# Kernel optimization log

Hardware: AMD Instinct MI355X
Metric: run time of the kernel (lower is better)

## Reference

```python
import jax, jax.numpy as jnp
import numpy as np

EPS = 1e-5

def _quant_w(w):
    # symmetric per-tensor 8-bit weight quantization with straight-through estimator
    s = jnp.max(jnp.abs(w)) / 127.0
    wq = jnp.round(jnp.clip(w / s, -127.0, 127.0)) * s
    return w + jax.lax.stop_gradient(wq - w)

def _adder_conv(x, w, stride):
    # AdderNet conv: out[b,co,ow] = -sum_{cin,k} |x[b,cin,ow*stride+k] - w[co,cin,k]|
    # x: (B, Cin, L), w: (Co, Cin, K)
    B, Cin, L = x.shape
    Co, _, K = w.shape
    Ow = (L - K) // stride + 1
    idx = jnp.arange(Ow)[:, None] * stride + jnp.arange(K)[None, :]      # (Ow, K)
    patches = x[:, :, idx]                                               # (B, Cin, Ow, K)
    diff = jnp.abs(patches[:, None] - w[None, :, :, None, :])            # (B, Co, Cin, Ow, K)
    return -diff.sum(axis=(2, 4))                                        # (B, Co, Ow)

def _bn(x, p):
    # eval-mode BatchNorm; x: (B,C,W), p: (4,C) = [gamma, beta, running_mean, running_var]
    g, b, m, v = p
    return (x - m[:, None]) * (g[:, None] * jax.lax.rsqrt(v[:, None] + EPS)) + b[:, None]

def _bn_params(key, c):
    k1, k2, k3, k4 = jax.random.split(key, 4)
    g = jax.random.uniform(k1, (c,)) + 0.5
    b = 0.1 * jax.random.normal(k2, (c,))
    m = 0.1 * jax.random.normal(k3, (c,))
    v = jax.random.uniform(k4, (c,)) + 0.5
    return jnp.stack([g, b, m, v]).astype(jnp.float32)

def setup_inputs() -> dict:
    key = jax.random.key(0)
    ks = jax.random.split(key, 22)
    B = 8192
    w = lambda k, shp: (0.1 * jax.random.normal(k, shp)).astype(jnp.float32)
    return {
        'x': jax.random.normal(ks[0], (B, 1, 1, 256), dtype=jnp.float32),
        'w_pre1': w(ks[1], (5, 1, 13)),   'bn_pre1': _bn_params(ks[2], 5),
        'w_pre2': w(ks[3], (10, 5, 9)),   'bn_pre2': _bn_params(ks[4], 10),
        'w_r1':   w(ks[5], (10, 10, 1)),  'bn_r1':   _bn_params(ks[6], 10),
        'w_r2':   w(ks[7], (10, 10, 1)),  'bn_r2':   _bn_params(ks[8], 10),
        'w_o1a':  w(ks[9], (70, 140, 1)), 'bn_o1a':  _bn_params(ks[10], 70),
        'w_o1b':  w(ks[11], (30, 70, 1)), 'bn_o1b':  _bn_params(ks[12], 30),
        'w_o1c':  w(ks[13], (1, 30, 1)),  'bn_o1c':  _bn_params(ks[14], 1),
        'w_o2a':  w(ks[15], (70, 140, 1)),'bn_o2a':  _bn_params(ks[16], 70),
        'w_o2b':  w(ks[17], (30, 70, 1)), 'bn_o2b':  _bn_params(ks[18], 30),
        'w_o2c':  w(ks[19], (1, 30, 1)),  'bn_o2c':  _bn_params(ks[20], 1),
    }

def reference(x, w_pre1, bn_pre1, w_pre2, bn_pre2, w_r1, bn_r1, w_r2, bn_r2,
              w_o1a, bn_o1a, w_o1b, bn_o1b, w_o1c, bn_o1c,
              w_o2a, bn_o2a, w_o2b, bn_o2b, w_o2c, bn_o2c):
    relu = jax.nn.relu
    B = x.shape[0]
    h = x.reshape(B, 1, 256)                                  # height dim is 1 -> 1D
    h = relu(_bn(_adder_conv(h, _quant_w(w_pre1), 5), bn_pre1))   # (B,5,49)
    h = relu(_bn(_adder_conv(h, _quant_w(w_pre2), 3), bn_pre2))   # (B,10,14)
    # ResBlock
    t = relu(_bn(_adder_conv(h, _quant_w(w_r1), 1), bn_r1))
    t = _bn(_adder_conv(t, _quant_w(w_r2), 1), bn_r2)
    h = relu(t + h)                                           # (B,10,14)
    f = h.reshape(B, 140, 1)                                  # flatten to channels
    # O1 branch (amplitude-weighted average lifetime)
    a = relu(_bn(_adder_conv(f, _quant_w(w_o1a), 1), bn_o1a))
    a = relu(_bn(_adder_conv(a, _quant_w(w_o1b), 1), bn_o1b))
    a = relu(_bn(_adder_conv(a, _quant_w(w_o1c), 1), bn_o1c))
    tau_amp = a.reshape(-1)                                   # (B,)
    # O2 branch (intensity-weighted average lifetime)
    b = relu(_bn(_adder_conv(f, _quant_w(w_o2a), 1), bn_o2a))
    b = relu(_bn(_adder_conv(b, _quant_w(w_o2b), 1), bn_o2b))
    b = relu(_bn(_adder_conv(b, _quant_w(w_o2c), 1), bn_o2c))
    tau_inten = b.reshape(-1)                                 # (B,)
    return (tau_amp, tau_inten)
```

## Files before the change

### kernel.cpp

```cpp
#include <hip/hip_runtime.h>

#define TPB 256
#define EPB 8
#define H1S 246
#define ES  280

#define WQ1   0
#define WQ2   65
#define WR1Q  515
#define WR2Q  615
#define WCQ   715
#define WSB   779
#define SMALL_N 1253
#define WQAT  1280
#define WQBT  20880

#define SB_P1 0
#define SB_P2 10
#define SB_R1 30
#define SB_R2 50
#define SB_A1 70
#define SB_B1 210
#define SB_C1 270
#define SB_A2 272
#define SB_B2 412
#define SB_C2 472

#define GFOLD(bn, C, OFF)                                                     \
  if (tid < (C)) {                                                            \
    float gg = (bn)[tid], bb = (bn)[(C) + tid];                               \
    float mm = (bn)[2 * (C) + tid], vv = (bn)[3 * (C) + tid];                 \
    float sc = gg / sqrtf(vv + 1e-5f);                                        \
    sbp[(OFF) + tid] = sc;                                                    \
    sbp[(OFF) + (C) + tid] = bb - mm * sc;                                    \
  }

extern "C" __global__ __launch_bounds__(256)
void prep(const float* __restrict__ w1,  const float* __restrict__ bnp1,
          const float* __restrict__ w2,  const float* __restrict__ bnp2,
          const float* __restrict__ wr1, const float* __restrict__ bnr1,
          const float* __restrict__ wr2, const float* __restrict__ bnr2,
          const float* __restrict__ wa1, const float* __restrict__ bna1,
          const float* __restrict__ wb1, const float* __restrict__ bnb1,
          const float* __restrict__ wc1, const float* __restrict__ bnc1,
          const float* __restrict__ wa2, const float* __restrict__ bna2,
          const float* __restrict__ wb2, const float* __restrict__ bnb2,
          const float* __restrict__ wc2, const float* __restrict__ bnc2,
          float* __restrict__ ws)
{
  __shared__ float s_red[4];
  const int tid = threadIdx.x;
  const int b = blockIdx.x;

  if (b == 10) {
    float* sbp = ws + WSB;
    GFOLD(bnp1, 5, SB_P1)  GFOLD(bnp2, 10, SB_P2)
    GFOLD(bnr1, 10, SB_R1) GFOLD(bnr2, 10, SB_R2)
    GFOLD(bna1, 70, SB_A1) GFOLD(bnb1, 30, SB_B1) GFOLD(bnc1, 1, SB_C1)
    GFOLD(bna2, 70, SB_A2) GFOLD(bnb2, 30, SB_B2) GFOLD(bnc2, 1, SB_C2)
    return;
  }

  const float* src; int n; int mode; int rofs; float* dst = ws;
  int ofs = 0;
  switch (b) {
    case 0: src = w1;  ofs = WQ1;      n = 65;   mode = 0; rofs = 0;  break;
    case 1: src = w2;  ofs = WQ2;      n = 450;  mode = 0; rofs = 0;  break;
    case 2: src = wr1; ofs = WR1Q;     n = 100;  mode = 0; rofs = 0;  break;
    case 3: src = wr2; ofs = WR2Q;     n = 100;  mode = 0; rofs = 0;  break;
    case 4: src = wa1; ofs = WQAT;     n = 9800; mode = 1; rofs = 0;  break;
    case 5: src = wb1; ofs = WQBT;     n = 2100; mode = 2; rofs = 0;  break;
    case 6: src = wc1; ofs = WCQ;      n = 30;   mode = 0; rofs = 0;  break;
    case 7: src = wa2; ofs = WQAT;     n = 9800; mode = 1; rofs = 70; break;
    case 8: src = wb2; ofs = WQBT;     n = 2100; mode = 2; rofs = 30; break;
    default:src = wc2; ofs = WCQ + 32; n = 30;   mode = 0; rofs = 0;  break;
  }

  const int n4 = n >> 2;
  const float4* s4 = (const float4*)src;

  float m = 0.f;
  for (int i = tid; i < n4; i += 256) {
    float4 v = s4[i];
    m = fmaxf(m, fmaxf(fmaxf(fabsf(v.x), fabsf(v.y)),
                       fmaxf(fabsf(v.z), fabsf(v.w))));
  }
  for (int i = (n4 << 2) + tid; i < n; i += 256) m = fmaxf(m, fabsf(src[i]));
#pragma unroll
  for (int off = 32; off > 0; off >>= 1)
    m = fmaxf(m, __shfl_down(m, off, 64));
  if ((tid & 63) == 0) s_red[tid >> 6] = m;
  __syncthreads();
  m = fmaxf(fmaxf(s_red[0], s_red[1]), fmaxf(s_red[2], s_red[3]));

  const float s = m / 127.0f;
  auto qz = [&](float w) {
    return rintf(fminf(fmaxf(w / s, -127.f), 127.f)) * s;
  };

  if (mode == 0) {
    for (int i = tid; i < n4; i += 256) {
      float4 v = s4[i];
      int base = 4 * i;
      dst[ofs + base]     = qz(v.x);
      dst[ofs + base + 1] = qz(v.y);
      dst[ofs + base + 2] = qz(v.z);
      dst[ofs + base + 3] = qz(v.w);
    }
    for (int i = (n4 << 2) + tid; i < n; i += 256) dst[ofs + i] = qz(src[i]);
  } else if (mode == 1) {
    for (int i = tid; i < n4; i += 256) {
      float4 v = s4[i];
      int base = 4 * i;
      int r = base / 140 + rofs, c = base % 140;
      float4 q4;
      q4.x = qz(v.x); q4.y = qz(v.y); q4.z = qz(v.z); q4.w = qz(v.w);
      *(float4*)&dst[ofs + ((c >> 2) * 140 + r) * 4] = q4;
    }
  } else {
    for (int i = tid; i < n4; i += 256) {
      float4 v = s4[i];
      int base = 4 * i;
      float q[4] = {qz(v.x), qz(v.y), qz(v.z), qz(v.w)};
#pragma unroll
      for (int cpt = 0; cpt < 4; ++cpt) {
        int ii = base + cpt;
        int r = ii / 70 + rofs, c = ii % 70;
        dst[ofs + ((c >> 1) * 60 + r) * 2 + (c & 1)] = q[cpt];
      }
    }
  }
}

extern "C" __global__ __launch_bounds__(TPB, 4)
void taunet(const float* __restrict__ x, const float* __restrict__ ws,
            float* __restrict__ out, int B)
{
  __shared__ __align__(16) float s_h1[EPB * H1S];
  __shared__ __align__(16) float s_e[EPB * ES];
  __shared__ __align__(16) float s_small[SMALL_N];

  const int tid = threadIdx.x;
  const int g  = tid >> 5;
  const int l  = tid & 31;
  const int ln = tid & 63;
  const int wv = tid >> 6;
  const int gp = 2 * wv;
  const int elem = blockIdx.x * EPB + g;

  {
    const float4* w4p = (const float4*)ws;
    for (int i = ln; i < (SMALL_N >> 2); i += 64)
      *(float4*)&s_small[i * 4] = w4p[i];
    if (ln == 0) s_small[1252] = ws[1252];
  }

  {
    const float4* xb = (const float4*)x;
#pragma unroll
    for (int it = 0; it < 2; ++it) {
      int e = gp + it;
      int ge = blockIdx.x * EPB + e;
      if (ge < B) {
        float4 v = xb[ge * 64 + ln];
        *(float4*)&s_e[e * ES + ln * 4] = v;
      }
    }
  }

  const float* sb = &s_small[WSB];

  {
    const float* xe = &s_e[g * ES];
#pragma unroll
    for (int rep = 0; rep < 2; ++rep) {
      int p = l + 32 * rep;
      bool act = p < 49;
      int ps = act ? p : 0;
      float win[13];
#pragma unroll
      for (int k = 0; k < 13; ++k) win[k] = xe[5 * ps + k];
#pragma unroll
      for (int ci = 0; ci < 5; ++ci) {
        float a0 = 0.f, a1 = 0.f;
#pragma unroll
        for (int k = 0; k < 13; ++k) {
          float d = fabsf(win[k] - ws[WQ1 + ci * 13 + k]);
          if (k & 1) a1 += d; else a0 += d;
        }
        float v = fmaxf(fmaf(-(a0 + a1), ws[WSB + SB_P1 + ci],
                             ws[WSB + SB_P1 + 5 + ci]), 0.f);
        if (act) s_h1[g * H1S + ci * 49 + ps] = v;
      }
    }
  }

  {
    const int ch = l >> 4;
    const int ow16 = l & 15;
    const bool act = ow16 < 14;
    const int ow = act ? ow16 : 0;
    const float* h1b = &s_h1[g * H1S];
    float acc[5] = {0.f, 0.f, 0.f, 0.f, 0.f};
#pragma unroll
    for (int ci = 0; ci < 5; ++ci) {
      float w9[9];
#pragma unroll
      for (int k = 0; k < 9; ++k) w9[k] = h1b[ci * 49 + 3 * ow + k];
#pragma unroll
      for (int c = 0; c < 5; ++c) {
        int co = ch * 5 + c;
        float s0 = 0.f, s1 = 0.f;
#pragma unroll
        for (int k = 0; k < 9; ++k) {
          float d = fabsf(w9[k] - s_small[WQ2 + co * 45 + ci * 9 + k]);
          if (k & 1) s1 += d; else s0 += d;
        }
        acc[c] += s0 + s1;
      }
    }
#pragma unroll
    for (int c = 0; c < 5; ++c) {
      int co = ch * 5 + c;
      float v = fmaxf(fmaf(-acc[c], sb[SB_P2 + co], sb[SB_P2 + 10 + co]), 0.f);
      if (act) s_e[g * ES + co * 14 + ow] = v;
    }
  }

#pragma unroll
  for (int j = 0; j < 5; ++j) {
    int idx = l + 32 * j;
    if (idx < 140) {
      int co = idx / 14, ow = idx % 14;
      float a0 = 0.f, a1 = 0.f;
#pragma unroll
      for (int ci = 0; ci < 10; ++ci) {
        float d = fabsf(s_e[g * ES + ci * 14 + ow] - s_small[WR1Q + co * 10 + ci]);
        if (ci & 1) a1 += d; else a0 += d;
      }
      s_e[g * ES + 140 + idx] =
          fmaxf(fmaf(-(a0 + a1), sb[SB_R1 + co], sb[SB_R1 + 10 + co]), 0.f);
    }
  }

#pragma unroll
  for (int j = 0; j < 5; ++j) {
    int idx = l + 32 * j;
    if (idx < 140) {
      int co = idx / 14, ow = idx % 14;
      float a0 = 0.f, a1 = 0.f;
#pragma unroll
      for (int ci = 0; ci < 10; ++ci) {
        float d = fabsf(s_e[g * ES + 140 + ci * 14 + ow] - s_small[WR2Q + co * 10 + ci]);
        if (ci & 1) a1 += d; else a0 += d;
      }
      float t2 = fmaf(-(a0 + a1), sb[SB_R2 + co], sb[SB_R2 + 10 + co]);
      s_e[g * ES + idx] = fmaxf(t2 + s_e[g * ES + idx], 0.f);
    }
  }

  __syncthreads();

  {
    const int rh = wv >> 1;
    const int eh = wv & 1;
    const int e0 = eh * 4;
    const int rbase = rh * 70;
    const float* hbp[4] = {&s_e[(e0 + 0) * ES], &s_e[(e0 + 1) * ES],
                           &s_e[(e0 + 2) * ES], &s_e[(e0 + 3) * ES]};
    const int q1 = ln / 6;
    const int rm = ln - q1 * 6;
    const bool act1 = ln < 24;
    const int row1 = rbase + 64 + (act1 ? rm : 0);
    const float* hb1p = hbp[act1 ? q1 : 0];

    float acc0[4][4], acc1[4];
#pragma unroll
    for (int e = 0; e < 4; ++e)
#pragma unroll
      for (int j = 0; j < 4; ++j) acc0[e][j] = 0.f;
#pragma unroll
    for (int j = 0; j < 4; ++j) acc1[j] = 0.f;

#pragma unroll 2
    for (int cb = 0; cb < 35; ++cb) {
      float4 w0 = *(const float4*)&ws[WQAT + (cb * 140 + rbase + ln) * 4];
      float4 w1 = *(const float4*)&ws[WQAT + (cb * 140 + row1) * 4];
#pragma unroll
      for (int e = 0; e < 4; ++e) {
        float4 h4 = *(const float4*)&hbp[e][cb * 4];
        acc0[e][0] += fabsf(h4.x - w0.x);
        acc0[e][1] += fabsf(h4.y - w0.y);
        acc0[e][2] += fabsf(h4.z - w0.z);
        acc0[e][3] += fabsf(h4.w - w0.w);
      }
      float4 p4 = *(const float4*)&hb1p[cb * 4];
      acc1[0] += fabsf(p4.x - w1.x);
      acc1[1] += fabsf(p4.y - w1.y);
      acc1[2] += fabsf(p4.z - w1.z);
      acc1[3] += fabsf(p4.w - w1.w);
    }

    {
      int off = rh ? SB_A2 : SB_A1;
      float sc = sb[off + ln], bi = sb[off + 70 + ln];
#pragma unroll
      for (int e = 0; e < 4; ++e) {
        float sad = (acc0[e][0] + acc0[e][1]) + (acc0[e][2] + acc0[e][3]);
        s_h1[(e0 + e) * H1S + rbase + ln] = fmaxf(fmaf(-sad, sc, bi), 0.f);
      }
    }
    if (act1) {
      int off = rh ? SB_A2 : SB_A1;
      int co = 64 + rm;
      float sc = sb[off + co], bi = sb[off + 70 + co];
      float sad = (acc1[0] + acc1[1]) + (acc1[2] + acc1[3]);
      s_h1[(e0 + q1) * H1S + rbase + 64 + rm] = fmaxf(fmaf(-sad, sc, bi), 0.f);
    }
  }

  __syncthreads();

  {
    const int brh = wv >> 1;
    const int e0 = (wv & 1) * 4;
    const bool act = ln < 30;
    const int rl = act ? ln : 0;
    const int rr = brh * 30 + rl;
    const float* h0p = &s_h1[(e0 + 0) * H1S + brh * 70];
    const float* h1p = &s_h1[(e0 + 1) * H1S + brh * 70];
    const float* h2p = &s_h1[(e0 + 2) * H1S + brh * 70];
    const float* h3p = &s_h1[(e0 + 3) * H1S + brh * 70];
    const int off = brh ? SB_B2 : SB_B1;
    float a0 = 0.f, a1 = 0.f, b0 = 0.f, b1 = 0.f,
          c0 = 0.f, c1 = 0.f, d0 = 0.f, d1 = 0.f;
#pragma unroll 7
    for (int ci = 0; ci < 35; ++ci) {
      float2 w2v = *(const float2*)&ws[WQBT + (ci * 60 + rr) * 2];
      float2 h0v = *(const float2*)&h0p[2 * ci];
      float2 h1v = *(const float2*)&h1p[2 * ci];
      float2 h2v = *(const float2*)&h2p[2 * ci];
      float2 h3v = *(const float2*)&h3p[2 * ci];
      a0 += fabsf(h0v.x - w2v.x);  a1 += fabsf(h0v.y - w2v.y);
      b0 += fabsf(h1v.x - w2v.x);  b1 += fabsf(h1v.y - w2v.y);
      c0 += fabsf(h2v.x - w2v.x);  c1 += fabsf(h2v.y - w2v.y);
      d0 += fabsf(h3v.x - w2v.x);  d1 += fabsf(h3v.y - w2v.y);
    }
    if (act) {
      float sc = sb[off + rl], bi = sb[off + 30 + rl];
      s_e[(e0 + 0) * ES + 140 + rr] = fmaxf(fmaf(-(a0 + a1), sc, bi), 0.f);
      s_e[(e0 + 1) * ES + 140 + rr] = fmaxf(fmaf(-(b0 + b1), sc, bi), 0.f);
      s_e[(e0 + 2) * ES + 140 + rr] = fmaxf(fmaf(-(c0 + c1), sc, bi), 0.f);
      s_e[(e0 + 3) * ES + 140 + rr] = fmaxf(fmaf(-(d0 + d1), sc, bi), 0.f);
    }
  }

  __syncthreads();

  for (int br = 0; br < 2; ++br) {
    float d = 0.f;
    if (l < 30)
      d = fabsf(s_e[g * ES + 140 + br * 30 + l] - s_small[WCQ + br * 32 + l]);
#pragma unroll
    for (int off = 16; off > 0; off >>= 1)
      d += __shfl_down(d, off, 32);
    if (l == 0 && elem < B) {
      int sbC = br ? SB_C2 : SB_C1;
      out[br * B + elem] = fmaxf(fmaf(-d, sb[sbC], sb[sbC + 1]), 0.f);
    }
  }
}

extern "C" void kernel_launch(void* const* d_in, const int* in_sizes, int n_in,
                              void* d_out, int out_size, void* d_ws, size_t ws_size,
                              hipStream_t stream) {
  const float* x    = (const float*)d_in[0];
  const float* w1   = (const float*)d_in[1];
  const float* bnp1 = (const float*)d_in[2];
  const float* w2   = (const float*)d_in[3];
  const float* bnp2 = (const float*)d_in[4];
  const float* wr1  = (const float*)d_in[5];
  const float* bnr1 = (const float*)d_in[6];
  const float* wr2  = (const float*)d_in[7];
  const float* bnr2 = (const float*)d_in[8];
  const float* wa1  = (const float*)d_in[9];
  const float* bna1 = (const float*)d_in[10];
  const float* wb1  = (const float*)d_in[11];
  const float* bnb1 = (const float*)d_in[12];
  const float* wc1  = (const float*)d_in[13];
  const float* bnc1 = (const float*)d_in[14];
  const float* wa2  = (const float*)d_in[15];
  const float* bna2 = (const float*)d_in[16];
  const float* wb2  = (const float*)d_in[17];
  const float* bnb2 = (const float*)d_in[18];
  const float* wc2  = (const float*)d_in[19];
  const float* bnc2 = (const float*)d_in[20];

  float* ws = (float*)d_ws;
  int B = in_sizes[0] / 256;
  int blocks = (B + EPB - 1) / EPB;

  hipLaunchKernelGGL(prep, dim3(11), dim3(256), 0, stream,
                     w1, bnp1, w2, bnp2, wr1, bnr1, wr2, bnr2,
                     wa1, bna1, wb1, bnb1, wc1, bnc1,
                     wa2, bna2, wb2, bnb2, wc2, bnc2, ws);

  hipLaunchKernelGGL(taunet, dim3(blocks), dim3(TPB), 0, stream,
                     x, ws, (float*)d_out, B);
}
```

Baseline: 137.0 us.

## Halve elements per block and remap threads to one wavefront per element

Cuts the batch elements per block from 8 to 4 and gives each 64-lane wavefront one element in the early conv stages, instead of one 32-lane half-wave per element. The dense stages are re-split so each thread handles two elements, or one element for the second layer, rather than four. Launch bounds request 8 blocks per SM to raise occupancy. The trade-off is that each weight value loaded from global memory in the dense layers is now reused across fewer elements, so weight traffic per element roughly doubles, and lanes sit idle in stages 2 and 3.

```diff
diff --git a/kernel.cpp b/kernel.cpp
--- a/kernel.cpp
+++ b/kernel.cpp
@@ -1,7 +1,7 @@
 #include <hip/hip_runtime.h>
 
 #define TPB 256
-#define EPB 8
+#define EPB 4
 #define H1S 246
 #define ES  280
 
@@ -132,7 +132,7 @@
   }
 }
 
-extern "C" __global__ __launch_bounds__(TPB, 4)
+extern "C" __global__ __launch_bounds__(TPB, 8)
 void taunet(const float* __restrict__ x, const float* __restrict__ ws,
             float* __restrict__ out, int B)
 {
@@ -141,12 +141,9 @@
   __shared__ __align__(16) float s_small[SMALL_N];
 
   const int tid = threadIdx.x;
-  const int g  = tid >> 5;
-  const int l  = tid & 31;
   const int ln = tid & 63;
   const int wv = tid >> 6;
-  const int gp = 2 * wv;
-  const int elem = blockIdx.x * EPB + g;
+  const int elem = blockIdx.x * EPB + wv;
 
   {
     const float4* w4p = (const float4*)ws;
@@ -155,107 +152,102 @@
     if (ln == 0) s_small[1252] = ws[1252];
   }
 
-  {
+  if (elem < B) {
     const float4* xb = (const float4*)x;
-#pragma unroll
-    for (int it = 0; it < 2; ++it) {
-      int e = gp + it;
-      int ge = blockIdx.x * EPB + e;
-      if (ge < B) {
-        float4 v = xb[ge * 64 + ln];
-        *(float4*)&s_e[e * ES + ln * 4] = v;
-      }
-    }
+    float4 v = xb[elem * 64 + ln];
+    *(float4*)&s_e[wv * ES + ln * 4] = v;
   }
 
   const float* sb = &s_small[WSB];
 
   {
-    const float* xe = &s_e[g * ES];
-#pragma unroll
-    for (int rep = 0; rep < 2; ++rep) {
-      int p = l + 32 * rep;
-      bool act = p < 49;
-      int ps = act ? p : 0;
-      float win[13];
-#pragma unroll
-      for (int k = 0; k < 13; ++k) win[k] = xe[5 * ps + k];
-#pragma unroll
-      for (int ci = 0; ci < 5; ++ci) {
-        float a0 = 0.f, a1 = 0.f;
-#pragma unroll
-        for (int k = 0; k < 13; ++k) {
-          float d = fabsf(win[k] - ws[WQ1 + ci * 13 + k]);
-          if (k & 1) a1 += d; else a0 += d;
-        }
-        float v = fmaxf(fmaf(-(a0 + a1), ws[WSB + SB_P1 + ci],
-                             ws[WSB + SB_P1 + 5 + ci]), 0.f);
-        if (act) s_h1[g * H1S + ci * 49 + ps] = v;
-      }
-    }
-  }
-
-  {
-    const int ch = l >> 4;
-    const int ow16 = l & 15;
+    const float* xe = &s_e[wv * ES];
+    const bool act = ln < 49;
+    const int ps = act ? ln : 0;
+    float win[13];
+#pragma unroll
+    for (int k = 0; k < 13; ++k) win[k] = xe[5 * ps + k];
+#pragma unroll
+    for (int ci = 0; ci < 5; ++ci) {
+      float a0 = 0.f, a1 = 0.f;
+#pragma unroll
+      for (int k = 0; k < 13; ++k) {
+        float d = fabsf(win[k] - ws[WQ1 + ci * 13 + k]);
+        if (k & 1) a1 += d; else a0 += d;
+      }
+      float v = fmaxf(fmaf(-(a0 + a1), ws[WSB + SB_P1 + ci],
+                           ws[WSB + SB_P1 + 5 + ci]), 0.f);
+      if (act) s_h1[wv * H1S + ci * 49 + ps] = v;
+    }
+  }
+
+  {
+    const int ch4 = ln >> 4;
+    const int ow16 = ln & 15;
     const bool act = ow16 < 14;
     const int ow = act ? ow16 : 0;
-    const float* h1b = &s_h1[g * H1S];
-    float acc[5] = {0.f, 0.f, 0.f, 0.f, 0.f};
+    const float* h1b = &s_h1[wv * H1S];
+    float acc[3] = {0.f, 0.f, 0.f};
+    int cos[3]; bool cact[3];
+#pragma unroll
+    for (int c = 0; c < 3; ++c) {
+      int co = ch4 + 4 * c;
+      cact[c] = act && (co < 10);
+      cos[c] = co < 10 ? co : 9;
+    }
 #pragma unroll
     for (int ci = 0; ci < 5; ++ci) {
       float w9[9];
 #pragma unroll
       for (int k = 0; k < 9; ++k) w9[k] = h1b[ci * 49 + 3 * ow + k];
 #pragma unroll
-      for (int c = 0; c < 5; ++c) {
-        int co = ch * 5 + c;
+      for (int c = 0; c < 3; ++c) {
         float s0 = 0.f, s1 = 0.f;
 #pragma unroll
         for (int k = 0; k < 9; ++k) {
-          float d = fabsf(w9[k] - s_small[WQ2 + co * 45 + ci * 9 + k]);
+          float d = fabsf(w9[k] - s_small[WQ2 + cos[c] * 45 + ci * 9 + k]);
           if (k & 1) s1 += d; else s0 += d;
         }
         acc[c] += s0 + s1;
       }
     }
 #pragma unroll
-    for (int c = 0; c < 5; ++c) {
-      int co = ch * 5 + c;
+    for (int c = 0; c < 3; ++c) {
+      int co = cos[c];
       float v = fmaxf(fmaf(-acc[c], sb[SB_P2 + co], sb[SB_P2 + 10 + co]), 0.f);
-      if (act) s_e[g * ES + co * 14 + ow] = v;
-    }
-  }
-
-#pragma unroll
-  for (int j = 0; j < 5; ++j) {
-    int idx = l + 32 * j;
+      if (cact[c]) s_e[wv * ES + co * 14 + ow] = v;
+    }
+  }
+
+#pragma unroll
+  for (int j = 0; j < 3; ++j) {
+    int idx = ln + 64 * j;
     if (idx < 140) {
       int co = idx / 14, ow = idx % 14;
       float a0 = 0.f, a1 = 0.f;
 #pragma unroll
       for (int ci = 0; ci < 10; ++ci) {
-        float d = fabsf(s_e[g * ES + ci * 14 + ow] - s_small[WR1Q + co * 10 + ci]);
+        float d = fabsf(s_e[wv * ES + ci * 14 + ow] - s_small[WR1Q + co * 10 + ci]);
         if (ci & 1) a1 += d; else a0 += d;
       }
-      s_e[g * ES + 140 + idx] =
+      s_e[wv * ES + 140 + idx] =
           fmaxf(fmaf(-(a0 + a1), sb[SB_R1 + co], sb[SB_R1 + 10 + co]), 0.f);
     }
   }
 
 #pragma unroll
-  for (int j = 0; j < 5; ++j) {
-    int idx = l + 32 * j;
+  for (int j = 0; j < 3; ++j) {
+    int idx = ln + 64 * j;
     if (idx < 140) {
       int co = idx / 14, ow = idx % 14;
       float a0 = 0.f, a1 = 0.f;
 #pragma unroll
       for (int ci = 0; ci < 10; ++ci) {
-        float d = fabsf(s_e[g * ES + 140 + ci * 14 + ow] - s_small[WR2Q + co * 10 + ci]);
+        float d = fabsf(s_e[wv * ES + 140 + ci * 14 + ow] - s_small[WR2Q + co * 10 + ci]);
         if (ci & 1) a1 += d; else a0 += d;
       }
       float t2 = fmaf(-(a0 + a1), sb[SB_R2 + co], sb[SB_R2 + 10 + co]);
-      s_e[g * ES + idx] = fmaxf(t2 + s_e[g * ES + idx], 0.f);
+      s_e[wv * ES + idx] = fmaxf(t2 + s_e[wv * ES + idx], 0.f);
     }
   }
 
@@ -264,37 +256,35 @@
   {
     const int rh = wv >> 1;
     const int eh = wv & 1;
-    const int e0 = eh * 4;
+    const int ea = 2 * eh, eb = 2 * eh + 1;
     const int rbase = rh * 70;
-    const float* hbp[4] = {&s_e[(e0 + 0) * ES], &s_e[(e0 + 1) * ES],
-                           &s_e[(e0 + 2) * ES], &s_e[(e0 + 3) * ES]};
-    const int q1 = ln / 6;
-    const int rm = ln - q1 * 6;
-    const bool act1 = ln < 24;
-    const int row1 = rbase + 64 + (act1 ? rm : 0);
-    const float* hb1p = hbp[act1 ? q1 : 0];
-
-    float acc0[4][4], acc1[4];
-#pragma unroll
-    for (int e = 0; e < 4; ++e)
-#pragma unroll
-      for (int j = 0; j < 4; ++j) acc0[e][j] = 0.f;
-#pragma unroll
-    for (int j = 0; j < 4; ++j) acc1[j] = 0.f;
+    const float* ha = &s_e[ea * ES];
+    const float* hbq = &s_e[eb * ES];
+    const int q1 = (ln >= 6) ? 1 : 0;
+    const bool act1 = ln < 12;
+    const int rm = act1 ? (ln - 6 * q1) : 0;
+    const int row1 = rbase + 64 + rm;
+    const float* hb1p = (q1 && act1) ? hbq : ha;
+
+    float accA[4], accB[4], acc1[4];
+#pragma unroll
+    for (int j = 0; j < 4; ++j) { accA[j] = 0.f; accB[j] = 0.f; acc1[j] = 0.f; }
 
 #pragma unroll 2
     for (int cb = 0; cb < 35; ++cb) {
       float4 w0 = *(const float4*)&ws[WQAT + (cb * 140 + rbase + ln) * 4];
       float4 w1 = *(const float4*)&ws[WQAT + (cb * 140 + row1) * 4];
-#pragma unroll
-      for (int e = 0; e < 4; ++e) {
-        float4 h4 = *(const float4*)&hbp[e][cb * 4];
-        acc0[e][0] += fabsf(h4.x - w0.x);
-        acc0[e][1] += fabsf(h4.y - w0.y);
-        acc0[e][2] += fabsf(h4.z - w0.z);
-        acc0[e][3] += fabsf(h4.w - w0.w);
-      }
+      float4 h4 = *(const float4*)&ha[cb * 4];
+      float4 k4 = *(const float4*)&hbq[cb * 4];
       float4 p4 = *(const float4*)&hb1p[cb * 4];
+      accA[0] += fabsf(h4.x - w0.x);
+      accA[1] += fabsf(h4.y - w0.y);
+      accA[2] += fabsf(h4.z - w0.z);
+      accA[3] += fabsf(h4.w - w0.w);
+      accB[0] += fabsf(k4.x - w0.x);
+      accB[1] += fabsf(k4.y - w0.y);
+      accB[2] += fabsf(k4.z - w0.z);
+      accB[3] += fabsf(k4.w - w0.w);
       acc1[0] += fabsf(p4.x - w1.x);
       acc1[1] += fabsf(p4.y - w1.y);
       acc1[2] += fabsf(p4.z - w1.z);
@@ -304,18 +294,18 @@
     {
       int off = rh ? SB_A2 : SB_A1;
       float sc = sb[off + ln], bi = sb[off + 70 + ln];
-#pragma unroll
-      for (int e = 0; e < 4; ++e) {
-        float sad = (acc0[e][0] + acc0[e][1]) + (acc0[e][2] + acc0[e][3]);
-        s_h1[(e0 + e) * H1S + rbase + ln] = fmaxf(fmaf(-sad, sc, bi), 0.f);
-      }
+      float sadA = (accA[0] + accA[1]) + (accA[2] + accA[3]);
+      float sadB = (accB[0] + accB[1]) + (accB[2] + accB[3]);
+      s_h1[ea * H1S + rbase + ln] = fmaxf(fmaf(-sadA, sc, bi), 0.f);
+      s_h1[eb * H1S + rbase + ln] = fmaxf(fmaf(-sadB, sc, bi), 0.f);
     }
     if (act1) {
       int off = rh ? SB_A2 : SB_A1;
       int co = 64 + rm;
       float sc = sb[off + co], bi = sb[off + 70 + co];
       float sad = (acc1[0] + acc1[1]) + (acc1[2] + acc1[3]);
-      s_h1[(e0 + q1) * H1S + rbase + 64 + rm] = fmaxf(fmaf(-sad, sc, bi), 0.f);
+      int e = q1 ? eb : ea;
+      s_h1[e * H1S + rbase + 64 + rm] = fmaxf(fmaf(-sad, sc, bi), 0.f);
     }
   }
 
@@ -323,48 +313,40 @@
 
   {
     const int brh = wv >> 1;
-    const int e0 = (wv & 1) * 4;
-    const bool act = ln < 30;
-    const int rl = act ? ln : 0;
+    const int ehl = ln >> 5;
+    const int e = 2 * (wv & 1) + ehl;
+    const int l32 = ln & 31;
+    const bool act = l32 < 30;
+    const int rl = act ? l32 : 0;
     const int rr = brh * 30 + rl;
-    const float* h0p = &s_h1[(e0 + 0) * H1S + brh * 70];
-    const float* h1p = &s_h1[(e0 + 1) * H1S + brh * 70];
-    const float* h2p = &s_h1[(e0 + 2) * H1S + brh * 70];
-    const float* h3p = &s_h1[(e0 + 3) * H1S + brh * 70];
+    const float* hp = &s_h1[e * H1S + brh * 70];
     const int off = brh ? SB_B2 : SB_B1;
-    float a0 = 0.f, a1 = 0.f, b0 = 0.f, b1 = 0.f,
-          c0 = 0.f, c1 = 0.f, d0 = 0.f, d1 = 0.f;
+    float a0 = 0.f, a1 = 0.f;
 #pragma unroll 7
     for (int ci = 0; ci < 35; ++ci) {
       float2 w2v = *(const float2*)&ws[WQBT + (ci * 60 + rr) * 2];
-      float2 h0v = *(const float2*)&h0p[2 * ci];
-      float2 h1v = *(const float2*)&h1p[2 * ci];
-      float2 h2v = *(const float2*)&h2p[2 * ci];
-      float2 h3v = *(const float2*)&h3p[2 * ci];
-      a0 += fabsf(h0v.x - w2v.x);  a1 += fabsf(h0v.y - w2v.y);
-      b0 += fabsf(h1v.x - w2v.x);  b1 += fabsf(h1v.y - w2v.y);
-      c0 += fabsf(h2v.x - w2v.x);  c1 += fabsf(h2v.y - w2v.y);
-      d0 += fabsf(h3v.x - w2v.x);  d1 += fabsf(h3v.y - w2v.y);
+      float2 hv = *(const float2*)&hp[2 * ci];
+      a0 += fabsf(hv.x - w2v.x);
+      a1 += fabsf(hv.y - w2v.y);
     }
     if (act) {
       float sc = sb[off + rl], bi = sb[off + 30 + rl];
-      s_e[(e0 + 0) * ES + 140 + rr] = fmaxf(fmaf(-(a0 + a1), sc, bi), 0.f);
-      s_e[(e0 + 1) * ES + 140 + rr] = fmaxf(fmaf(-(b0 + b1), sc, bi), 0.f);
-      s_e[(e0 + 2) * ES + 140 + rr] = fmaxf(fmaf(-(c0 + c1), sc, bi), 0.f);
-      s_e[(e0 + 3) * ES + 140 + rr] = fmaxf(fmaf(-(d0 + d1), sc, bi), 0.f);
+      s_e[e * ES + 140 + rr] = fmaxf(fmaf(-(a0 + a1), sc, bi), 0.f);
     }
   }
 
   __syncthreads();
 
-  for (int br = 0; br < 2; ++br) {
+  {
+    const int br = ln >> 5;
+    const int l32 = ln & 31;
     float d = 0.f;
-    if (l < 30)
-      d = fabsf(s_e[g * ES + 140 + br * 30 + l] - s_small[WCQ + br * 32 + l]);
+    if (l32 < 30)
+      d = fabsf(s_e[wv * ES + 140 + br * 30 + l32] - s_small[WCQ + br * 32 + l32]);
 #pragma unroll
     for (int off = 16; off > 0; off >>= 1)
       d += __shfl_down(d, off, 32);
-    if (l == 0 && elem < B) {
+    if (l32 == 0 && elem < B) {
       int sbC = br ? SB_C2 : SB_C1;
       out[br * B + elem] = fmaxf(fmaf(-d, sb[sbC], sb[sbC + 1]), 0.f);
     }
```

Result: slower. 175.0 us (+27.7%).
